# Kernel tuning notes

Measured on AMD Instinct MI355X. Metric: run time of the kernel, lower is better.

The kernel has to match this reference:

```python
import jax, jax.numpy as jnp
import numpy as np

NUM_HEADS = 12

def _pe(L, d):
    # standard sinusoidal positional encoding, shape (1, L, d)
    pos = jnp.arange(L, dtype=jnp.float32)[:, None]
    i = jnp.arange(d)[None, :]
    angle = pos / jnp.power(10000.0, (2 * (i // 2)).astype(jnp.float32) / d)
    pe = jnp.where(i % 2 == 0, jnp.sin(angle), jnp.cos(angle))
    return pe[None]

def _ln(x, scale, bias, eps=1e-5):
    m = x.mean(-1, keepdims=True)
    v = ((x - m) ** 2).mean(-1, keepdims=True)
    return (x - m) / jnp.sqrt(v + eps) * scale + bias

def setup_inputs() -> dict:
    key = jax.random.key(0)
    ks = jax.random.split(key, 8)
    D = 768
    s = 0.02
    return {
        "x": jax.random.normal(ks[0], (8, D, 32, 32), jnp.float32),
        "context_token": jax.random.normal(ks[1], (1, 1, D), jnp.float32),
        "register_tokens": jax.random.normal(ks[2], (1, 4, D), jnp.float32),
        "in_proj_w": jax.random.normal(ks[3], (3 * D, D), jnp.float32) * s,
        "in_proj_b": jnp.zeros((3 * D,), jnp.float32),
        "out_proj_w": jax.random.normal(ks[4], (D, D), jnp.float32) * s,
        "out_proj_b": jnp.zeros((D,), jnp.float32),
        "ln1_s": jnp.ones((D,), jnp.float32),
        "ln1_b": jnp.zeros((D,), jnp.float32),
        "ln2_s": jnp.ones((D,), jnp.float32),
        "ln2_b": jnp.zeros((D,), jnp.float32),
        "ffn_w1": jax.random.normal(ks[5], (4 * D, D), jnp.float32) * s,
        "ffn_b1": jnp.zeros((4 * D,), jnp.float32),
        "ffn_w2": jax.random.normal(ks[6], (D, 4 * D), jnp.float32) * s,
        "ffn_b2": jnp.zeros((D,), jnp.float32),
    }

def reference(x, context_token, register_tokens, in_proj_w, in_proj_b,
              out_proj_w, out_proj_b, ln1_s, ln1_b, ln2_s, ln2_b,
              ffn_w1, ffn_b1, ffn_w2, ffn_b2):
    B, d, h, w = x.shape
    N = h * w
    R = register_tokens.shape[1]
    G = 1 + R  # global tokens: context + registers
    nh = NUM_HEADS
    dh = d // nh
    # (B, N, d)
    x_flat = x.reshape(B, d, N).transpose(0, 2, 1)
    tokens = jnp.concatenate([
        jnp.broadcast_to(context_token, (B, 1, d)),
        jnp.broadcast_to(register_tokens, (B, R, d)),
    ], axis=1)
    tokens = tokens + _pe(G, d)
    xwt = _ln(jnp.concatenate([tokens, x_flat], axis=1), ln1_s, ln1_b)
    S = G + N
    # MultiheadAttention (eval mode, dropout off): fused in-projection
    qkv = xwt @ in_proj_w.T + in_proj_b
    q, k, v = jnp.split(qkv, 3, axis=-1)
    to_heads = lambda t: t.reshape(B, S, nh, dh).transpose(0, 2, 1, 3)
    q, k, v = to_heads(q), to_heads(k), to_heads(v)
    scores = jnp.einsum('bhqd,bhkd->bhqk', q, k) / np.float32(np.sqrt(dh))
    # mask (True = disallowed): feature rows (>=G) cannot attend to global cols (<G);
    # global rows attend everything; feature-feature block allowed.
    row_feat = jnp.arange(S) >= G
    col_glob = jnp.arange(S) < G
    disallowed = row_feat[:, None] & col_glob[None, :]
    scores = jnp.where(disallowed, -jnp.inf, scores)
    attn = jax.nn.softmax(scores, axis=-1)
    o = jnp.einsum('bhqk,bhkd->bhqd', attn, v).transpose(0, 2, 1, 3).reshape(B, S, d)
    o = o @ out_proj_w.T + out_proj_b
    y = o + xwt
    ff = jax.nn.gelu(_ln(y, ln2_s, ln2_b) @ ffn_w1.T + ffn_b1, approximate=False) @ ffn_w2.T + ffn_b2
    y = y + ff
    context_out = y[:, 0:1, :]
    register_out = y[:, 1:G, :]
    feature_out = y[:, G:, :].transpose(0, 2, 1).reshape(B, d, h, w)
    return feature_out, context_out, register_out
```

## Files before the change

### kernel.cpp

```cpp
#include <hip/hip_runtime.h>
#include <hip/hip_bf16.h>
#include <cmath>

typedef unsigned short u16;
typedef __bf16 bf16x8 __attribute__((ext_vector_type(8)));
typedef float floatx4 __attribute__((ext_vector_type(4)));

#define SQ 1029
#define DM 768
#define NH 12
#define SQP 1088
#define SSC 0.18033688011112042f

#define GLD16(gp, lp) __builtin_amdgcn_global_load_lds( \
    (const __attribute__((address_space(1))) unsigned int*)(gp), \
    (__attribute__((address_space(3))) unsigned int*)(lp), 16, 0, 0)

#define OFF_WQKV ((size_t)0)
#define OFF_WOUT ((size_t)3538944)
#define OFF_W1   ((size_t)4718592)
#define OFF_W2   ((size_t)9437184)
#define OFF_XF   ((size_t)14155776)
#define OFF_XWT  ((size_t)26800128)
#define OFF_QKV  ((size_t)39444480)
#define OFF_VT   ((size_t)77783040)
#define OFF_Y    ((size_t)91152384)
#define OFF_BQ   ((size_t)103796736)

__device__ __forceinline__ float bf2f(u16 u) {
  unsigned int x = ((unsigned int)u) << 16;
  float f; __builtin_memcpy(&f, &x, 4); return f;
}
__device__ __forceinline__ u16 f2bf(float f) {
  unsigned int x; __builtin_memcpy(&x, &f, 4);
  x = (x + 0x7fffu + ((x >> 16) & 1u)) >> 16;
  return (u16)x;
}
__device__ __forceinline__ unsigned int pk_bf16(float a, float b) {
  __hip_bfloat162 h = __float22bfloat162_rn(make_float2(a, b));
  unsigned int u; __builtin_memcpy(&u, &h, 4); return u;
}

__device__ __forceinline__ void blockReduce2(float& s1, float& s2) {
  #pragma unroll
  for (int o = 32; o > 0; o >>= 1) { s1 += __shfl_xor(s1, o); s2 += __shfl_xor(s2, o); }
  __shared__ float t1[4], t2[4];
  const int w = threadIdx.x >> 6;
  if ((threadIdx.x & 63) == 0) { t1[w] = s1; t2[w] = s2; }
  __syncthreads();
  s1 = t1[0] + t1[1] + t1[2] + t1[3];
  s2 = t2[0] + t2[1] + t2[2] + t2[3];
}

__global__ __launch_bounds__(256) void convw_all(
    const float* __restrict__ a, const float* __restrict__ b,
    const float* __restrict__ c, const float* __restrict__ d, u16* __restrict__ dst) {
  int i = blockIdx.x * 256 + threadIdx.x;
  if (i >= 1769472) return;
  const float* src; int off;
  if (i < 442368)       { src = a; off = i; }
  else if (i < 589824)  { src = b; off = i - 442368; }
  else if (i < 1179648) { src = c; off = i - 589824; }
  else                  { src = d; off = i - 1179648; }
  float4 v = ((const float4*)src)[off];
  if (i < 147456) { v.x *= SSC; v.y *= SSC; v.z *= SSC; v.w *= SSC; }
  ushort4 o; o.x = f2bf(v.x); o.y = f2bf(v.y); o.z = f2bf(v.z); o.w = f2bf(v.w);
  ((ushort4*)dst)[i] = o;
}

__global__ __launch_bounds__(256) void convb(const float* __restrict__ b, float* __restrict__ o) {
  int i = blockIdx.x * 256 + threadIdx.x;
  if (i >= 2304) return;
  o[i] = (i < 768) ? b[i] * SSC : b[i];
}

__global__ __launch_bounds__(256) void transpose_x(const float* __restrict__ x, u16* __restrict__ xf) {
  __shared__ u16 tile[32][33];
  const int b = blockIdx.x, ct = blockIdx.y, nt = blockIdx.z;
  const int i = threadIdx.x, jj = threadIdx.y;
  #pragma unroll
  for (int kk = 0; kk < 4; ++kk) {
    int j = jj + kk * 8;
    tile[j][i] = f2bf(x[((size_t)b * 768 + ct * 32 + j) * 1024 + nt * 32 + i]);
  }
  __syncthreads();
  #pragma unroll
  for (int kk = 0; kk < 4; ++kk) {
    int j = jj + kk * 8;
    xf[((size_t)b * 1024 + nt * 32 + j) * 768 + ct * 32 + i] = tile[i][j];
  }
}

__global__ __launch_bounds__(256) void build_xwt(
    const u16* __restrict__ xf, const float* __restrict__ ctx, const float* __restrict__ regt,
    const float* __restrict__ g, const float* __restrict__ be, u16* __restrict__ xwt) {
  const int row = blockIdx.x;
  const int b = row / SQ, s = row % SQ;
  const int tid = threadIdx.x;
  float v[3];
  #pragma unroll
  for (int i = 0; i < 3; ++i) {
    const int c = tid + i * 256;
    float val;
    if (s >= 5) {
      val = bf2f(xf[((size_t)b * 1024 + (s - 5)) * DM + c]);
    } else {
      float tok = (s == 0) ? ctx[c] : regt[(s - 1) * DM + c];
      float e = (float)(2 * (c / 2)) * (1.0f / 768.0f);
      float ang = (float)s / powf(10000.0f, e);
      val = tok + ((c & 1) ? cosf(ang) : sinf(ang));
    }
    v[i] = val;
  }
  float s1 = v[0] + v[1] + v[2];
  float s2 = v[0] * v[0] + v[1] * v[1] + v[2] * v[2];
  blockReduce2(s1, s2);
  const float mean = s1 * (1.0f / 768.0f);
  const float var = s2 * (1.0f / 768.0f) - mean * mean;
  const float rs = rsqrtf(fmaxf(var, 0.0f) + 1e-5f);
  #pragma unroll
  for (int i = 0; i < 3; ++i) {
    const int c = tid + i * 256;
    xwt[(size_t)row * DM + c] = f2bf((v[i] - mean) * rs * g[c] + be[c]);
  }
}

__global__ __launch_bounds__(256) void ln2k(
    const u16* __restrict__ y, const float* __restrict__ g, const float* __restrict__ be,
    u16* __restrict__ out) {
  const int row = blockIdx.x;
  const int tid = threadIdx.x;
  float v[3];
  #pragma unroll
  for (int i = 0; i < 3; ++i) v[i] = bf2f(y[(size_t)row * DM + tid + i * 256]);
  float s1 = v[0] + v[1] + v[2];
  float s2 = v[0] * v[0] + v[1] * v[1] + v[2] * v[2];
  blockReduce2(s1, s2);
  const float mean = s1 * (1.0f / 768.0f);
  const float var = s2 * (1.0f / 768.0f) - mean * mean;
  const float rs = rsqrtf(fmaxf(var, 0.0f) + 1e-5f);
  #pragma unroll
  for (int i = 0; i < 3; ++i) {
    const int c = tid + i * 256;
    out[(size_t)row * DM + c] = f2bf((v[i] - mean) * rs * g[c] + be[c]);
  }
}

template<int EPI, int K, int NB>
__global__ __launch_bounds__(256) void gemmk(
    const u16* __restrict__ A, const u16* __restrict__ W, const float* __restrict__ bias,
    const u16* __restrict__ res, u16* __restrict__ out, int M) {
  constexpr int N = NB * 128;
  __shared__ u16 SM[16384];
  u16* Asm = SM;
  u16* Bsm = SM + 8192;
  const int tid = threadIdx.x, wave = tid >> 6, lane = tid & 63, quad = lane >> 4, l16 = lane & 15;
  const int lin = blockIdx.x;
  constexpr int FULL = 64 * NB;
  int mb, nb;
  if (lin < FULL) { const int g = lin / (8 * NB); const int r = lin - g * 8 * NB; mb = g * 8 + (r & 7); nb = r >> 3; }
  else { mb = 64; nb = lin - FULL; }
  const int m0 = mb * 128, n0 = nb * 128;
  const int wm = wave & 1, wn = wave >> 1;

  const u16* Ap[4]; const u16* Wp[4]; u16* la[4]; u16* lb[4];
  #pragma unroll
  for (int it = 0; it < 4; ++it) {
    const int c = it * 256 + tid;
    const int row = c >> 3, gch = (c & 7) ^ (row & 7);
    Ap[it] = A + (size_t)min(m0 + row, M - 1) * K + gch * 8;
    Wp[it] = W + (size_t)(n0 + row) * K + gch * 8;
    la[it] = Asm + c * 8;
    lb[it] = Bsm + c * 8;
  }

  floatx4 acc[4][4];
  #pragma unroll
  for (int i = 0; i < 4; ++i)
    #pragma unroll
    for (int j = 0; j < 4; ++j) { floatx4 z = {0.f, 0.f, 0.f, 0.f}; acc[i][j] = z; }

  const int ch0 = (quad ^ (l16 & 7)) << 3;
  const int ch1 = ((4 + quad) ^ (l16 & 7)) << 3;

  #pragma unroll 1
  for (int ko = 0; ko < K / 768; ++ko) {
    #pragma unroll
    for (int ki = 0; ki < 768; ki += 64) {
      __syncthreads();
      #pragma unroll
      for (int it = 0; it < 4; ++it) GLD16(Ap[it] + ki, la[it]);
      #pragma unroll
      for (int it = 0; it < 4; ++it) GLD16(Wp[it] + ki, lb[it]);
      __syncthreads();
      #pragma unroll
      for (int kk = 0; kk < 2; ++kk) {
        const int ch = kk ? ch1 : ch0;
        bf16x8 a[4], b[4];
        #pragma unroll
        for (int i = 0; i < 4; ++i) a[i] = *(const bf16x8*)&Asm[(wm * 64 + i * 16 + l16) * 64 + ch];
        #pragma unroll
        for (int j = 0; j < 4; ++j) b[j] = *(const bf16x8*)&Bsm[(wn * 64 + j * 16 + l16) * 64 + ch];
        #pragma unroll
        for (int i = 0; i < 4; ++i)
          #pragma unroll
          for (int j = 0; j < 4; ++j)
            acc[i][j] = __builtin_amdgcn_mfma_f32_16x16x32_bf16(b[j], a[i], acc[i][j], 0, 0, 0);
      }
    }
    if (K > 768) {
      #pragma unroll
      for (int it = 0; it < 4; ++it) { Ap[it] += 768; Wp[it] += 768; }
    }
  }

  #pragma unroll
  for (int j = 0; j < 4; ++j) {
    const float4 b4 = *(const float4*)(bias + n0 + wn * 64 + j * 16 + quad * 4);
    #pragma unroll
    for (int i = 0; i < 4; ++i) {
      acc[i][j][0] += b4.x; acc[i][j][1] += b4.y; acc[i][j][2] += b4.z; acc[i][j][3] += b4.w;
    }
  }
  if constexpr (EPI == 2) {
    #pragma unroll
    for (int i = 0; i < 4; ++i)
      #pragma unroll
      for (int j = 0; j < 4; ++j)
        #pragma unroll
        for (int r = 0; r < 4; ++r) {
          const float v = acc[i][j][r];
          acc[i][j][r] = v / (1.0f + exp2f(-2.3022221f * (v + 0.044715f * v * v * v)));
        }
  }
  __syncthreads();
  u16* Ep = SM + wave * 2304;
  #pragma unroll
  for (int h = 0; h < 2; ++h) {
    #pragma unroll
    for (int i2 = 0; i2 < 2; ++i2) {
      const int i = h * 2 + i2;
      #pragma unroll
      for (int j = 0; j < 4; ++j) {
        uint2 w;
        w.x = pk_bf16(acc[i][j][0], acc[i][j][1]);
        w.y = pk_bf16(acc[i][j][2], acc[i][j][3]);
        *(uint2*)&Ep[(i2 * 16 + l16) * 72 + j * 16 + quad * 4] = w;
      }
    }
    #pragma unroll
    for (int s = 0; s < 4; ++s) {
      const int lrow = s * 8 + (lane >> 3);
      const int gm = m0 + wm * 64 + h * 32 + lrow;
      const int gn = n0 + wn * 64 + (lane & 7) * 8;
      uint4 lv = *(const uint4*)&Ep[lrow * 72 + (lane & 7) * 8];
      if constexpr (EPI == 1 || EPI == 3) {
        const uint4 rv = *(const uint4*)(res + (size_t)min(gm, M - 1) * N + gn);
        const unsigned* lp = &lv.x; const unsigned* rp = &rv.x;
        uint4 ov; unsigned* op = &ov.x;
        #pragma unroll
        for (int d = 0; d < 4; ++d) {
          const float a0 = bf2f((u16)(lp[d] & 0xffffu)) + bf2f((u16)(rp[d] & 0xffffu));
          const float a1 = bf2f((u16)(lp[d] >> 16)) + bf2f((u16)(rp[d] >> 16));
          op[d] = pk_bf16(a0, a1);
        }
        lv = ov;
      }
      if (gm < M) *(uint4*)(out + (size_t)gm * N + gn) = lv;
    }
  }
}

__global__ __launch_bounds__(256) void vtrans(const u16* __restrict__ qkv, u16* __restrict__ vt) {
  __shared__ u16 t[32][33];
  const int bh = blockIdx.x, st = blockIdx.y, dt = blockIdx.z;
  const int bq = bh / NH, hh = bh % NH;
  u16* vd = vt + (size_t)bh * 64 * SQP;
  const int i = threadIdx.x, jj = threadIdx.y;
  #pragma unroll
  for (int kk = 0; kk < 4; ++kk) {
    int j = jj + kk * 8;
    t[j][i] = qkv[(size_t)(bq * SQ + st * 32 + j) * 2304 + 1536 + hh * 64 + dt * 32 + i];
  }
  __syncthreads();
  #pragma unroll
  for (int kk = 0; kk < 4; ++kk) {
    int j = jj + kk * 8;
    vd[(size_t)(dt * 32 + j) * SQP + st * 32 + i] = t[i][j];
  }
}

__global__ __launch_bounds__(256) void attn_flash(
    const u16* __restrict__ qkv, const u16* __restrict__ vt, u16* __restrict__ out) {
  const int bh = blockIdx.x, qt = blockIdx.y;
  const int b = bh / NH, h = bh % NH;
  const int tid = threadIdx.x, wave = tid >> 6, lane = tid & 63, quad = lane >> 4, l16 = lane & 15;
  __shared__ u16 Qs[4096], Ks[4096], VTs[4096];
  __shared__ u16 Ps[64 * 72];
  const int q0 = qt * 64;
  const u16* qk = qkv + (size_t)b * SQ * 2304 + h * 64;
  const u16* vslab = vt + (size_t)bh * 64 * SQP;
  const int c0 = tid, c1 = tid + 256;
  const int r0 = c0 >> 3, q0c = (c0 & 7) ^ (r0 & 7);
  const int r1 = c1 >> 3, q1c = (c1 & 7) ^ (r1 & 7);
  u16* L0Q = Qs + wave * 512;  u16* L1Q = Qs + 2048 + wave * 512;
  u16* L0K = Ks + wave * 512;  u16* L1K = Ks + 2048 + wave * 512;
  u16* L0V = VTs + wave * 512; u16* L1V = VTs + 2048 + wave * 512;

  GLD16(qk + (size_t)(q0 + r0) * 2304 + q0c * 8, L0Q);
  GLD16(qk + (size_t)(q0 + r1) * 2304 + q1c * 8, L1Q);

  floatx4 Oa[4];
  #pragma unroll
  for (int nt = 0; nt < 4; ++nt) { floatx4 z = {0.f, 0.f, 0.f, 0.f}; Oa[nt] = z; }
  float l_acc = 0.f;
  const int qrow = wave * 16 + l16;
  const bool qfeat = (q0 + qrow >= 5);
  bf16x8 qf0, qf1;

  for (int t = 0; t < 17; ++t) {
    const int k0 = t * 64;
    __syncthreads();
    GLD16(qk + 768 + (size_t)(k0 + r0) * 2304 + q0c * 8, L0K);
    GLD16(qk + 768 + (size_t)(k0 + r1) * 2304 + q1c * 8, L1K);
    GLD16(vslab + (size_t)r0 * SQP + k0 + q0c * 8, L0V);
    GLD16(vslab + (size_t)r1 * SQP + k0 + q1c * 8, L1V);
    __syncthreads();

    if (t == 0) {
      qf0 = *(const bf16x8*)&Qs[qrow * 64 + ((quad ^ (qrow & 7)) << 3)];
      qf1 = *(const bf16x8*)&Qs[qrow * 64 + (((4 + quad) ^ (qrow & 7)) << 3)];
    }

    floatx4 st[4];
    #pragma unroll
    for (int mt = 0; mt < 4; ++mt) { floatx4 z = {0.f, 0.f, 0.f, 0.f}; st[mt] = z; }
    #pragma unroll
    for (int kk = 0; kk < 2; ++kk) {
      const bf16x8 qf = kk ? qf1 : qf0;
      #pragma unroll
      for (int mt = 0; mt < 4; ++mt) {
        const int krow = mt * 16 + l16;
        bf16x8 kf = *(const bf16x8*)&Ks[krow * 64 + (((kk * 4 + quad) ^ (krow & 7)) << 3)];
        st[mt] = __builtin_amdgcn_mfma_f32_16x16x32_bf16(kf, qf, st[mt], 0, 0, 0);
      }
    }

    if (t == 16) {
      float p[4];
      #pragma unroll
      for (int r = 0; r < 4; ++r) {
        float pv = exp2f(st[0][r]);
        p[r] = (quad * 4 + r < 5) ? pv : 0.f;
      }
      l_acc += (p[0] + p[1]) + (p[2] + p[3]);
      uint2 w;
      w.x = pk_bf16(p[0], p[1]);
      w.y = pk_bf16(p[2], p[3]);
      *(uint2*)&Ps[qrow * 72 + quad * 4] = w;
      const uint2 zz = {0u, 0u};
      #pragma unroll
      for (int mt = 1; mt < 4; ++mt) *(uint2*)&Ps[qrow * 72 + mt * 16 + quad * 4] = zz;
    } else if (t == 0) {
      #pragma unroll
      for (int mt = 0; mt < 4; ++mt) {
        float p[4];
        #pragma unroll
        for (int r = 0; r < 4; ++r) {
          float pv = exp2f(st[mt][r]);
          if (mt == 0) pv = (qfeat && (quad * 4 + r < 5)) ? 0.f : pv;
          p[r] = pv;
        }
        l_acc += (p[0] + p[1]) + (p[2] + p[3]);
        uint2 w;
        w.x = pk_bf16(p[0], p[1]);
        w.y = pk_bf16(p[2], p[3]);
        *(uint2*)&Ps[qrow * 72 + mt * 16 + quad * 4] = w;
      }
    } else {
      #pragma unroll
      for (int mt = 0; mt < 4; ++mt) {
        float p[4];
        #pragma unroll
        for (int r = 0; r < 4; ++r) p[r] = exp2f(st[mt][r]);
        l_acc += (p[0] + p[1]) + (p[2] + p[3]);
        uint2 w;
        w.x = pk_bf16(p[0], p[1]);
        w.y = pk_bf16(p[2], p[3]);
        *(uint2*)&Ps[qrow * 72 + mt * 16 + quad * 4] = w;
      }
    }

    auto pv_step = [&](int kk) {
      bf16x8 pf = *(const bf16x8*)&Ps[qrow * 72 + kk * 32 + quad * 8];
      #pragma unroll
      for (int nt = 0; nt < 4; ++nt) {
        const int brow = nt * 16 + l16;
        bf16x8 bb = *(const bf16x8*)&VTs[brow * 64 + (((kk * 4 + quad) ^ (brow & 7)) << 3)];
        Oa[nt] = __builtin_amdgcn_mfma_f32_16x16x32_bf16(pf, bb, Oa[nt], 0, 0, 0);
      }
    };
    pv_step(0);
    if (t != 16) pv_step(1);
  }

  float lt = l_acc;
  lt += __shfl_xor(lt, 16);
  lt += __shfl_xor(lt, 32);
  lt = fmaxf(lt, 1e-30f);
  #pragma unroll
  for (int nt = 0; nt < 4; ++nt)
    #pragma unroll
    for (int r = 0; r < 4; ++r) {
      const int qo = quad * 4 + r;
      const float lr = __shfl(lt, (lane & 48) | qo);
      const int qg2 = q0 + wave * 16 + qo;
      if (qg2 < SQ)
        out[((size_t)b * SQ + qg2) * DM + h * 64 + nt * 16 + l16] = f2bf(Oa[nt][r] / lr);
    }
}

__global__ __launch_bounds__(256) void transpose_out(const u16* __restrict__ yf, float* __restrict__ out) {
  __shared__ u16 tile[32][33];
  const int b = blockIdx.x, nt = blockIdx.y, ct = blockIdx.z;
  const int i = threadIdx.x, jj = threadIdx.y;
  #pragma unroll
  for (int kk = 0; kk < 4; ++kk) {
    int j = jj + kk * 8;
    tile[j][i] = yf[((size_t)b * SQ + 5 + nt * 32 + j) * DM + ct * 32 + i];
  }
  __syncthreads();
  #pragma unroll
  for (int kk = 0; kk < 4; ++kk) {
    int j = jj + kk * 8;
    out[((size_t)b * 768 + ct * 32 + j) * 1024 + nt * 32 + i] = bf2f(tile[i][j]);
  }
}

__global__ __launch_bounds__(256) void out_small(const u16* __restrict__ yf, float* __restrict__ out) {
  const int idx = blockIdx.x * 256 + threadIdx.x;
  if (idx >= 8 * 5 * DM) return;
  const int b = idx / (5 * DM);
  const int r = idx % (5 * DM);
  const int s = r / DM, c = r % DM;
  const float v = bf2f(yf[((size_t)b * SQ + s) * DM + c]);
  if (s == 0) out[(size_t)6291456 + (size_t)b * DM + c] = v;
  else out[(size_t)6291456 + 6144 + ((size_t)b * 4 + (s - 1)) * DM + c] = v;
}

extern "C" void kernel_launch(void* const* d_in, const int* in_sizes, int n_in,
                              void* d_out, int out_size, void* d_ws, size_t ws_size,
                              hipStream_t stream) {
  const float* x    = (const float*)d_in[0];
  const float* ctx  = (const float*)d_in[1];
  const float* regt = (const float*)d_in[2];
  const float* wqkv = (const float*)d_in[3];
  const float* bqkv = (const float*)d_in[4];
  const float* wout = (const float*)d_in[5];
  const float* bout = (const float*)d_in[6];
  const float* ln1s = (const float*)d_in[7];
  const float* ln1b = (const float*)d_in[8];
  const float* ln2s = (const float*)d_in[9];
  const float* ln2b = (const float*)d_in[10];
  const float* w1   = (const float*)d_in[11];
  const float* b1   = (const float*)d_in[12];
  const float* w2   = (const float*)d_in[13];
  const float* b2   = (const float*)d_in[14];

  char* ws = (char*)d_ws;
  u16* wb_all = (u16*)(ws + OFF_WQKV);
  u16* wqkv_b = (u16*)(ws + OFF_WQKV);
  u16* wout_b = (u16*)(ws + OFF_WOUT);
  u16* w1_b   = (u16*)(ws + OFF_W1);
  u16* w2_b   = (u16*)(ws + OFF_W2);
  u16* xf     = (u16*)(ws + OFF_XF);
  u16* xwt    = (u16*)(ws + OFF_XWT);
  u16* qkv    = (u16*)(ws + OFF_QKV);
  u16* vtb    = (u16*)(ws + OFF_VT);
  u16* yb     = (u16*)(ws + OFF_Y);
  float* bqs  = (float*)(ws + OFF_BQ);
  u16* attnb  = (u16*)(ws + OFF_XF);
  u16* ynorm  = (u16*)(ws + OFF_XF);
  u16* h1     = (u16*)(ws + OFF_QKV);
  u16* yfin   = (u16*)(ws + OFF_XWT);
  float* outp = (float*)d_out;

  convw_all   <<<6912, 256, 0, stream>>>(wqkv, wout, w1, w2, wb_all);
  convb       <<<9, 256, 0, stream>>>(bqkv, bqs);
  transpose_x <<<dim3(8, 24, 32), dim3(32, 8), 0, stream>>>(x, xf);
  build_xwt   <<<8232, 256, 0, stream>>>(xf, ctx, regt, ln1s, ln1b, xwt);
  gemmk<0, 768, 18><<<65 * 18, 256, 0, stream>>>(xwt, wqkv_b, bqs, nullptr, qkv, 8232);
  vtrans      <<<dim3(96, 34, 2), dim3(32, 8), 0, stream>>>(qkv, vtb);
  attn_flash  <<<dim3(96, 17), 256, 0, stream>>>(qkv, vtb, attnb);
  gemmk<1, 768, 6><<<65 * 6, 256, 0, stream>>>(attnb, wout_b, bout, xwt, yb, 8232);
  ln2k        <<<8232, 256, 0, stream>>>(yb, ln2s, ln2b, ynorm);
  gemmk<2, 768, 24><<<65 * 24, 256, 0, stream>>>(ynorm, w1_b, b1, nullptr, h1, 8232);
  gemmk<3, 3072, 6><<<65 * 6, 256, 0, stream>>>(h1, w2_b, b2, yb, yfin, 8232);
  transpose_out<<<dim3(8, 32, 24), dim3(32, 8), 0, stream>>>(yfin, outp);
  out_small   <<<120, 256, 0, stream>>>(yfin, outp);
}
```

Measured before the change: 399.1 us.

## Add 256x256-tile 512-thread GEMM with 4-stage LDS pipeline for QKV and FFN1

Adds a new GEMM kernel using 256x256 output tiles, 8 waves per block, a 4-slot direct-to-LDS load pipeline and 128 KB dynamic shared memory. It replaces the 128-wide tile kernel for the QKV projection and the first FFN layer. The larger tiles raise arithmetic intensity and cut redundant global loads. The cost is fewer blocks, hence worse wave quantization across CUs, and higher register and LDS pressure that may limit occupancy.

```diff
diff --git a/kernel.cpp b/kernel.cpp
--- a/kernel.cpp
+++ b/kernel.cpp
@@ -252,6 +252,133 @@
     for (int s = 0; s < 4; ++s) {
       const int lrow = s * 8 + (lane >> 3);
       const int gm = m0 + wm * 64 + h * 32 + lrow;
+      const int gn = n0 + wn * 64 + (lane & 7) * 8;
+      uint4 lv = *(const uint4*)&Ep[lrow * 72 + (lane & 7) * 8];
+      if constexpr (EPI == 1 || EPI == 3) {
+        const uint4 rv = *(const uint4*)(res + (size_t)min(gm, M - 1) * N + gn);
+        const unsigned* lp = &lv.x; const unsigned* rp = &rv.x;
+        uint4 ov; unsigned* op = &ov.x;
+        #pragma unroll
+        for (int d = 0; d < 4; ++d) {
+          const float a0 = bf2f((u16)(lp[d] & 0xffffu)) + bf2f((u16)(rp[d] & 0xffffu));
+          const float a1 = bf2f((u16)(lp[d] >> 16)) + bf2f((u16)(rp[d] >> 16));
+          op[d] = pk_bf16(a0, a1);
+        }
+        lv = ov;
+      }
+      if (gm < M) *(uint4*)(out + (size_t)gm * N + gn) = lv;
+    }
+  }
+}
+
+template<int EPI, int K, int NB>
+__global__ __launch_bounds__(512, 2) void gemm256(
+    const u16* __restrict__ A, const u16* __restrict__ W, const float* __restrict__ bias,
+    const u16* __restrict__ res, u16* __restrict__ out, int M) {
+  constexpr int N = NB * 256;
+  constexpr int NT = K / 32;
+  extern __shared__ __align__(16) char SMb[];
+  const int tid = threadIdx.x, wave = tid >> 6, lane = tid & 63, quad = lane >> 4, l16 = lane & 15;
+  const int wm = wave >> 2, wn = wave & 3;
+  const int lin = blockIdx.x;
+  int mb, nb;
+  if (lin < 32 * NB) { const int g = lin / (8 * NB); const int r = lin - g * 8 * NB; mb = g * 8 + (r & 7); nb = r >> 3; }
+  else { mb = 32; nb = lin - 32 * NB; }
+  const int m0 = mb * 256, n0 = nb * 256;
+
+  const u16* Ag[2]; const u16* Wg[2];
+  #pragma unroll
+  for (int it = 0; it < 2; ++it) {
+    const int c = it * 512 + tid;
+    const int row = c >> 2;
+    const int k8 = (c & 3) ^ (row & 3);
+    Ag[it] = A + (size_t)min(m0 + row, M - 1) * K + k8 * 8;
+    Wg[it] = W + (size_t)(n0 + row) * K + k8 * 8;
+  }
+  const int ldst = tid * 16;
+
+  floatx4 acc[8][4];
+  #pragma unroll
+  for (int i = 0; i < 8; ++i)
+    #pragma unroll
+    for (int j = 0; j < 4; ++j) { floatx4 z = {0.f, 0.f, 0.f, 0.f}; acc[i][j] = z; }
+
+  const int aoff = ((wm * 128 + l16) * 32 + ((quad ^ (l16 & 3)) << 3)) * 2;
+  const int boff = 65536 + ((wn * 64 + l16) * 32 + ((quad ^ (l16 & 3)) << 3)) * 2;
+
+  auto STAGE = [&](int ts, int slot) {
+    const size_t ko = (size_t)ts * 32;
+    char* ab = SMb + slot * 16384 + ldst;
+    char* bb = SMb + 65536 + slot * 16384 + ldst;
+    GLD16(Ag[0] + ko, ab);
+    GLD16(Ag[1] + ko, ab + 8192);
+    GLD16(Wg[0] + ko, bb);
+    GLD16(Wg[1] + ko, bb + 8192);
+  };
+
+  STAGE(0, 0); STAGE(1, 1); STAGE(2, 2);
+
+  #pragma unroll 1
+  for (int t = 0; t < NT; ++t) {
+    asm volatile("s_waitcnt vmcnt(8)" ::: "memory");
+    __builtin_amdgcn_s_barrier();
+    __builtin_amdgcn_sched_barrier(0);
+    STAGE(t + 3 < NT ? t + 3 : NT - 1, (t + 3) & 3);
+    const char* base = SMb + (t & 3) * 16384;
+    bf16x8 a[8], b[4];
+    #pragma unroll
+    for (int i = 0; i < 8; ++i) a[i] = *(const bf16x8*)(base + aoff + i * 1024);
+    #pragma unroll
+    for (int j = 0; j < 4; ++j) b[j] = *(const bf16x8*)(base + boff + j * 1024);
+    __builtin_amdgcn_s_setprio(1);
+    #pragma unroll
+    for (int i = 0; i < 8; ++i)
+      #pragma unroll
+      for (int j = 0; j < 4; ++j)
+        acc[i][j] = __builtin_amdgcn_mfma_f32_16x16x32_bf16(b[j], a[i], acc[i][j], 0, 0, 0);
+    __builtin_amdgcn_s_setprio(0);
+  }
+
+  asm volatile("s_waitcnt vmcnt(0)" ::: "memory");
+  __builtin_amdgcn_s_barrier();
+
+  #pragma unroll
+  for (int j = 0; j < 4; ++j) {
+    const float4 b4 = *(const float4*)(bias + n0 + wn * 64 + j * 16 + quad * 4);
+    #pragma unroll
+    for (int i = 0; i < 8; ++i) {
+      acc[i][j][0] += b4.x; acc[i][j][1] += b4.y; acc[i][j][2] += b4.z; acc[i][j][3] += b4.w;
+    }
+  }
+  if constexpr (EPI == 2) {
+    #pragma unroll
+    for (int i = 0; i < 8; ++i)
+      #pragma unroll
+      for (int j = 0; j < 4; ++j)
+        #pragma unroll
+        for (int r = 0; r < 4; ++r) {
+          const float v = acc[i][j][r];
+          acc[i][j][r] = v / (1.0f + exp2f(-2.3022221f * (v + 0.044715f * v * v * v)));
+        }
+  }
+  u16* Ep = (u16*)SMb + wave * 2304;
+  #pragma unroll
+  for (int g = 0; g < 4; ++g) {
+    #pragma unroll
+    for (int i2 = 0; i2 < 2; ++i2) {
+      const int i = g * 2 + i2;
+      #pragma unroll
+      for (int j = 0; j < 4; ++j) {
+        uint2 w;
+        w.x = pk_bf16(acc[i][j][0], acc[i][j][1]);
+        w.y = pk_bf16(acc[i][j][2], acc[i][j][3]);
+        *(uint2*)&Ep[(i2 * 16 + l16) * 72 + j * 16 + quad * 4] = w;
+      }
+    }
+    #pragma unroll
+    for (int s = 0; s < 4; ++s) {
+      const int lrow = s * 8 + (lane >> 3);
+      const int gm = m0 + wm * 128 + g * 32 + lrow;
       const int gn = n0 + wn * 64 + (lane & 7) * 8;
       uint4 lv = *(const uint4*)&Ep[lrow * 72 + (lane & 7) * 8];
       if constexpr (EPI == 1 || EPI == 3) {
@@ -485,16 +612,25 @@
   u16* yfin   = (u16*)(ws + OFF_XWT);
   float* outp = (float*)d_out;
 
+  static bool attr_done = false;
+  if (!attr_done) {
+    attr_done = true;
+    hipFuncSetAttribute(reinterpret_cast<const void*>(&gemm256<0, 768, 9>),
+                        hipFuncAttributeMaxDynamicSharedMemorySize, 131072);
+    hipFuncSetAttribute(reinterpret_cast<const void*>(&gemm256<2, 768, 12>),
+                        hipFuncAttributeMaxDynamicSharedMemorySize, 131072);
+  }
+
   convw_all   <<<6912, 256, 0, stream>>>(wqkv, wout, w1, w2, wb_all);
   convb       <<<9, 256, 0, stream>>>(bqkv, bqs);
   transpose_x <<<dim3(8, 24, 32), dim3(32, 8), 0, stream>>>(x, xf);
   build_xwt   <<<8232, 256, 0, stream>>>(xf, ctx, regt, ln1s, ln1b, xwt);
-  gemmk<0, 768, 18><<<65 * 18, 256, 0, stream>>>(xwt, wqkv_b, bqs, nullptr, qkv, 8232);
+  gemm256<0, 768, 9><<<33 * 9, 512, 131072, stream>>>(xwt, wqkv_b, bqs, nullptr, qkv, 8232);
   vtrans      <<<dim3(96, 34, 2), dim3(32, 8), 0, stream>>>(qkv, vtb);
   attn_flash  <<<dim3(96, 17), 256, 0, stream>>>(qkv, vtb, attnb);
   gemmk<1, 768, 6><<<65 * 6, 256, 0, stream>>>(attnb, wout_b, bout, xwt, yb, 8232);
   ln2k        <<<8232, 256, 0, stream>>>(yb, ln2s, ln2b, ynorm);
-  gemmk<2, 768, 24><<<65 * 24, 256, 0, stream>>>(ynorm, w1_b, b1, nullptr, h1, 8232);
+  gemm256<2, 768, 12><<<33 * 12, 512, 131072, stream>>>(ynorm, w1_b, b1, nullptr, h1, 8232);
   gemmk<3, 3072, 6><<<65 * 6, 256, 0, stream>>>(h1, w2_b, b2, yb, yfin, 8232);
   transpose_out<<<dim3(8, 32, 24), dim3(32, 8), 0, stream>>>(yfin, outp);
   out_small   <<<120, 256, 0, stream>>>(yfin, outp);
```

Result: slower. 412.8 us (+3.4%).

## Replace 128x128 GEMM with 256x256-tile double-buffered 8-wave GEMM

Applied to the files above, without the earlier changes.

Replaces the 128x128-tile, 4-wave, single-buffered GEMM with a 256x256-tile, 8-wave kernel that uses 128KB of dynamic LDS. Global-to-LDS loads for the next k-tiles are issued two stages ahead, waited on with explicit vmcnt counts, and MFMA sections are raised in priority with setprio. The goal is more data reuse per tile and overlap of memory loads with compute. The trade-off is far fewer blocks per GEMM (e.g. 99 for the out-projection and FFN2 GEMMs), which can leave many CUs idle on a large GPU and worsens tail effects from the partial last M tile.

```diff
diff --git a/kernel.cpp b/kernel.cpp
--- a/kernel.cpp
+++ b/kernel.cpp
@@ -147,84 +147,100 @@
 }
 
 template<int EPI, int K, int NB>
-__global__ __launch_bounds__(256) void gemmk(
+__global__ __launch_bounds__(512, 2) void gemm256(
     const u16* __restrict__ A, const u16* __restrict__ W, const float* __restrict__ bias,
     const u16* __restrict__ res, u16* __restrict__ out, int M) {
-  constexpr int N = NB * 128;
-  __shared__ u16 SM[16384];
-  u16* Asm = SM;
-  u16* Bsm = SM + 8192;
+  constexpr int N = NB * 256;
+  constexpr int NT = K / 64;
+  extern __shared__ __align__(16) char SMb[];
   const int tid = threadIdx.x, wave = tid >> 6, lane = tid & 63, quad = lane >> 4, l16 = lane & 15;
+  const int wm = wave >> 2, wn = wave & 3;
   const int lin = blockIdx.x;
-  constexpr int FULL = 64 * NB;
   int mb, nb;
-  if (lin < FULL) { const int g = lin / (8 * NB); const int r = lin - g * 8 * NB; mb = g * 8 + (r & 7); nb = r >> 3; }
-  else { mb = 64; nb = lin - FULL; }
-  const int m0 = mb * 128, n0 = nb * 128;
-  const int wm = wave & 1, wn = wave >> 1;
-
-  const u16* Ap[4]; const u16* Wp[4]; u16* la[4]; u16* lb[4];
+  if (lin < 32 * NB) { const int g = lin / (8 * NB); const int r = lin - g * 8 * NB; mb = g * 8 + (r & 7); nb = r >> 3; }
+  else { mb = 32; nb = lin - 32 * NB; }
+  const int m0 = mb * 256, n0 = nb * 256;
+
+  const u16* Ap[4]; const u16* Wp[4];
   #pragma unroll
   for (int it = 0; it < 4; ++it) {
-    const int c = it * 256 + tid;
+    const int c = it * 512 + tid;
     const int row = c >> 3, gch = (c & 7) ^ (row & 7);
     Ap[it] = A + (size_t)min(m0 + row, M - 1) * K + gch * 8;
     Wp[it] = W + (size_t)(n0 + row) * K + gch * 8;
-    la[it] = Asm + c * 8;
-    lb[it] = Bsm + c * 8;
-  }
-
-  floatx4 acc[4][4];
-  #pragma unroll
-  for (int i = 0; i < 4; ++i)
+  }
+  char* asl = SMb + tid * 16;
+  char* bsl = SMb + 65536 + tid * 16;
+
+  auto STAGE = [&](int ts, int slot) {
+    const int ko = ts * 64;
+    #pragma unroll
+    for (int it = 0; it < 4; ++it) GLD16(Ap[it] + ko, asl + slot * 32768 + it * 8192);
+    #pragma unroll
+    for (int it = 0; it < 4; ++it) GLD16(Wp[it] + ko, bsl + slot * 32768 + it * 8192);
+  };
+
+  floatx4 acc[8][4];
+  #pragma unroll
+  for (int i = 0; i < 8; ++i)
     #pragma unroll
     for (int j = 0; j < 4; ++j) { floatx4 z = {0.f, 0.f, 0.f, 0.f}; acc[i][j] = z; }
 
   const int ch0 = (quad ^ (l16 & 7)) << 3;
   const int ch1 = ((4 + quad) ^ (l16 & 7)) << 3;
 
+  STAGE(0, 0); STAGE(1, 1);
+
   #pragma unroll 1
-  for (int ko = 0; ko < K / 768; ++ko) {
-    #pragma unroll
-    for (int ki = 0; ki < 768; ki += 64) {
-      __syncthreads();
-      #pragma unroll
-      for (int it = 0; it < 4; ++it) GLD16(Ap[it] + ki, la[it]);
-      #pragma unroll
-      for (int it = 0; it < 4; ++it) GLD16(Wp[it] + ki, lb[it]);
-      __syncthreads();
-      #pragma unroll
-      for (int kk = 0; kk < 2; ++kk) {
-        const int ch = kk ? ch1 : ch0;
-        bf16x8 a[4], b[4];
-        #pragma unroll
-        for (int i = 0; i < 4; ++i) a[i] = *(const bf16x8*)&Asm[(wm * 64 + i * 16 + l16) * 64 + ch];
-        #pragma unroll
-        for (int j = 0; j < 4; ++j) b[j] = *(const bf16x8*)&Bsm[(wn * 64 + j * 16 + l16) * 64 + ch];
-        #pragma unroll
-        for (int i = 0; i < 4; ++i)
-          #pragma unroll
-          for (int j = 0; j < 4; ++j)
-            acc[i][j] = __builtin_amdgcn_mfma_f32_16x16x32_bf16(b[j], a[i], acc[i][j], 0, 0, 0);
-      }
-    }
-    if (K > 768) {
-      #pragma unroll
-      for (int it = 0; it < 4; ++it) { Ap[it] += 768; Wp[it] += 768; }
-    }
+  for (int t = 0; t < NT; ++t) {
+    if (t < NT - 1) { asm volatile("s_waitcnt vmcnt(8)" ::: "memory"); }
+    else            { asm volatile("s_waitcnt vmcnt(0)" ::: "memory"); }
+    __builtin_amdgcn_s_barrier();
+    __builtin_amdgcn_sched_barrier(0);
+    const u16* As = (const u16*)(SMb + (t & 1) * 32768);
+    const u16* Bs = (const u16*)(SMb + 65536 + (t & 1) * 32768);
+    bf16x8 a0[8], b0[4], a1[8], b1[4];
+    #pragma unroll
+    for (int i = 0; i < 8; ++i) a0[i] = *(const bf16x8*)&As[(wm * 128 + i * 16 + l16) * 64 + ch0];
+    #pragma unroll
+    for (int j = 0; j < 4; ++j) b0[j] = *(const bf16x8*)&Bs[(wn * 64 + j * 16 + l16) * 64 + ch0];
+    __builtin_amdgcn_s_setprio(1);
+    #pragma unroll
+    for (int i = 0; i < 8; ++i)
+      #pragma unroll
+      for (int j = 0; j < 4; ++j)
+        acc[i][j] = __builtin_amdgcn_mfma_f32_16x16x32_bf16(b0[j], a0[i], acc[i][j], 0, 0, 0);
+    __builtin_amdgcn_s_setprio(0);
+    #pragma unroll
+    for (int i = 0; i < 8; ++i) a1[i] = *(const bf16x8*)&As[(wm * 128 + i * 16 + l16) * 64 + ch1];
+    #pragma unroll
+    for (int j = 0; j < 4; ++j) b1[j] = *(const bf16x8*)&Bs[(wn * 64 + j * 16 + l16) * 64 + ch1];
+    asm volatile("s_waitcnt lgkmcnt(0)" ::: "memory");
+    __builtin_amdgcn_sched_barrier(0);
+    __builtin_amdgcn_s_barrier();
+    __builtin_amdgcn_sched_barrier(0);
+    if (t + 2 < NT) STAGE(t + 2, t & 1);
+    __builtin_amdgcn_sched_barrier(0);
+    __builtin_amdgcn_s_setprio(1);
+    #pragma unroll
+    for (int i = 0; i < 8; ++i)
+      #pragma unroll
+      for (int j = 0; j < 4; ++j)
+        acc[i][j] = __builtin_amdgcn_mfma_f32_16x16x32_bf16(b1[j], a1[i], acc[i][j], 0, 0, 0);
+    __builtin_amdgcn_s_setprio(0);
   }
 
   #pragma unroll
   for (int j = 0; j < 4; ++j) {
     const float4 b4 = *(const float4*)(bias + n0 + wn * 64 + j * 16 + quad * 4);
     #pragma unroll
-    for (int i = 0; i < 4; ++i) {
+    for (int i = 0; i < 8; ++i) {
       acc[i][j][0] += b4.x; acc[i][j][1] += b4.y; acc[i][j][2] += b4.z; acc[i][j][3] += b4.w;
     }
   }
   if constexpr (EPI == 2) {
     #pragma unroll
-    for (int i = 0; i < 4; ++i)
+    for (int i = 0; i < 8; ++i)
       #pragma unroll
       for (int j = 0; j < 4; ++j)
         #pragma unroll
@@ -233,13 +249,12 @@
           acc[i][j][r] = v / (1.0f + exp2f(-2.3022221f * (v + 0.044715f * v * v * v)));
         }
   }
-  __syncthreads();
-  u16* Ep = SM + wave * 2304;
-  #pragma unroll
-  for (int h = 0; h < 2; ++h) {
+  u16* Ep = (u16*)SMb + wave * 2304;
+  #pragma unroll
+  for (int g = 0; g < 4; ++g) {
     #pragma unroll
     for (int i2 = 0; i2 < 2; ++i2) {
-      const int i = h * 2 + i2;
+      const int i = g * 2 + i2;
       #pragma unroll
       for (int j = 0; j < 4; ++j) {
         uint2 w;
@@ -251,7 +266,7 @@
     #pragma unroll
     for (int s = 0; s < 4; ++s) {
       const int lrow = s * 8 + (lane >> 3);
-      const int gm = m0 + wm * 64 + h * 32 + lrow;
+      const int gm = m0 + wm * 128 + g * 32 + lrow;
       const int gn = n0 + wn * 64 + (lane & 7) * 8;
       uint4 lv = *(const uint4*)&Ep[lrow * 72 + (lane & 7) * 8];
       if constexpr (EPI == 1 || EPI == 3) {
@@ -485,17 +500,30 @@
   u16* yfin   = (u16*)(ws + OFF_XWT);
   float* outp = (float*)d_out;
 
+  static bool attr_done = false;
+  if (!attr_done) {
+    attr_done = true;
+    hipFuncSetAttribute(reinterpret_cast<const void*>(&gemm256<0, 768, 9>),
+                        hipFuncAttributeMaxDynamicSharedMemorySize, 131072);
+    hipFuncSetAttribute(reinterpret_cast<const void*>(&gemm256<1, 768, 3>),
+                        hipFuncAttributeMaxDynamicSharedMemorySize, 131072);
+    hipFuncSetAttribute(reinterpret_cast<const void*>(&gemm256<2, 768, 12>),
+                        hipFuncAttributeMaxDynamicSharedMemorySize, 131072);
+    hipFuncSetAttribute(reinterpret_cast<const void*>(&gemm256<3, 3072, 3>),
+                        hipFuncAttributeMaxDynamicSharedMemorySize, 131072);
+  }
+
   convw_all   <<<6912, 256, 0, stream>>>(wqkv, wout, w1, w2, wb_all);
   convb       <<<9, 256, 0, stream>>>(bqkv, bqs);
   transpose_x <<<dim3(8, 24, 32), dim3(32, 8), 0, stream>>>(x, xf);
   build_xwt   <<<8232, 256, 0, stream>>>(xf, ctx, regt, ln1s, ln1b, xwt);
-  gemmk<0, 768, 18><<<65 * 18, 256, 0, stream>>>(xwt, wqkv_b, bqs, nullptr, qkv, 8232);
+  gemm256<0, 768, 9><<<33 * 9, 512, 131072, stream>>>(xwt, wqkv_b, bqs, nullptr, qkv, 8232);
   vtrans      <<<dim3(96, 34, 2), dim3(32, 8), 0, stream>>>(qkv, vtb);
   attn_flash  <<<dim3(96, 17), 256, 0, stream>>>(qkv, vtb, attnb);
-  gemmk<1, 768, 6><<<65 * 6, 256, 0, stream>>>(attnb, wout_b, bout, xwt, yb, 8232);
+  gemm256<1, 768, 3><<<33 * 3, 512, 131072, stream>>>(attnb, wout_b, bout, xwt, yb, 8232);
   ln2k        <<<8232, 256, 0, stream>>>(yb, ln2s, ln2b, ynorm);
-  gemmk<2, 768, 24><<<65 * 24, 256, 0, stream>>>(ynorm, w1_b, b1, nullptr, h1, 8232);
-  gemmk<3, 3072, 6><<<65 * 6, 256, 0, stream>>>(h1, w2_b, b2, yb, yfin, 8232);
+  gemm256<2, 768, 12><<<33 * 12, 512, 131072, stream>>>(ynorm, w1_b, b1, nullptr, h1, 8232);
+  gemm256<3, 3072, 3><<<33 * 3, 512, 131072, stream>>>(h1, w2_b, b2, yb, yfin, 8232);
   transpose_out<<<dim3(8, 32, 24), dim3(32, 8), 0, stream>>>(yfin, outp);
   out_small   <<<120, 256, 0, stream>>>(yfin, outp);
 }
```

New measurement: 439.3 us. +10.1%, slower.

## Fuse input transpose with LayerNorm1 and fold bias conversion into weight kernel

Applied to the files above, without the earlier changes.

Replaces the separate transpose-to-bf16 kernel and the per-row LayerNorm kernel with one kernel that loads a 32-token slab of x, transposes it in shared memory and normalizes each row with wave-level reductions. This drops the bf16 intermediate round trip through global memory. Global tokens get their own small kernel, and the q-bias scaling is merged into the weight-conversion kernel to save a launch. The fused kernel uses about 49KB of LDS per block and runs only 256 blocks, which may limit occupancy.

```diff
diff --git a/kernel.cpp b/kernel.cpp
--- a/kernel.cpp
+++ b/kernel.cpp
@@ -54,9 +54,17 @@
 
 __global__ __launch_bounds__(256) void convw_all(
     const float* __restrict__ a, const float* __restrict__ b,
-    const float* __restrict__ c, const float* __restrict__ d, u16* __restrict__ dst) {
+    const float* __restrict__ c, const float* __restrict__ d,
+    const float* __restrict__ bq, u16* __restrict__ dst, float* __restrict__ bqs) {
   int i = blockIdx.x * 256 + threadIdx.x;
-  if (i >= 1769472) return;
+  if (i >= 1770048) return;
+  if (i >= 1769472) {
+    const int off = i - 1769472;
+    float4 v = ((const float4*)bq)[off];
+    if (off < 192) { v.x *= SSC; v.y *= SSC; v.z *= SSC; v.w *= SSC; }
+    ((float4*)bqs)[off] = v;
+    return;
+  }
   const float* src; int off;
   if (i < 442368)       { src = a; off = i; }
   else if (i < 589824)  { src = b; off = i - 442368; }
@@ -68,49 +76,20 @@
   ((ushort4*)dst)[i] = o;
 }
 
-__global__ __launch_bounds__(256) void convb(const float* __restrict__ b, float* __restrict__ o) {
-  int i = blockIdx.x * 256 + threadIdx.x;
-  if (i >= 2304) return;
-  o[i] = (i < 768) ? b[i] * SSC : b[i];
-}
-
-__global__ __launch_bounds__(256) void transpose_x(const float* __restrict__ x, u16* __restrict__ xf) {
-  __shared__ u16 tile[32][33];
-  const int b = blockIdx.x, ct = blockIdx.y, nt = blockIdx.z;
-  const int i = threadIdx.x, jj = threadIdx.y;
-  #pragma unroll
-  for (int kk = 0; kk < 4; ++kk) {
-    int j = jj + kk * 8;
-    tile[j][i] = f2bf(x[((size_t)b * 768 + ct * 32 + j) * 1024 + nt * 32 + i]);
-  }
-  __syncthreads();
-  #pragma unroll
-  for (int kk = 0; kk < 4; ++kk) {
-    int j = jj + kk * 8;
-    xf[((size_t)b * 1024 + nt * 32 + j) * 768 + ct * 32 + i] = tile[i][j];
-  }
-}
-
-__global__ __launch_bounds__(256) void build_xwt(
-    const u16* __restrict__ xf, const float* __restrict__ ctx, const float* __restrict__ regt,
+__global__ __launch_bounds__(256) void build_tok(
+    const float* __restrict__ ctx, const float* __restrict__ regt,
     const float* __restrict__ g, const float* __restrict__ be, u16* __restrict__ xwt) {
   const int row = blockIdx.x;
-  const int b = row / SQ, s = row % SQ;
+  const int b = row / 5, s = row % 5;
   const int tid = threadIdx.x;
   float v[3];
   #pragma unroll
   for (int i = 0; i < 3; ++i) {
     const int c = tid + i * 256;
-    float val;
-    if (s >= 5) {
-      val = bf2f(xf[((size_t)b * 1024 + (s - 5)) * DM + c]);
-    } else {
-      float tok = (s == 0) ? ctx[c] : regt[(s - 1) * DM + c];
-      float e = (float)(2 * (c / 2)) * (1.0f / 768.0f);
-      float ang = (float)s / powf(10000.0f, e);
-      val = tok + ((c & 1) ? cosf(ang) : sinf(ang));
-    }
-    v[i] = val;
+    float tok = (s == 0) ? ctx[c] : regt[(s - 1) * DM + c];
+    float e = (float)(2 * (c / 2)) * (1.0f / 768.0f);
+    float ang = (float)s / powf(10000.0f, e);
+    v[i] = tok + ((c & 1) ? cosf(ang) : sinf(ang));
   }
   float s1 = v[0] + v[1] + v[2];
   float s2 = v[0] * v[0] + v[1] * v[1] + v[2] * v[2];
@@ -121,7 +100,49 @@
   #pragma unroll
   for (int i = 0; i < 3; ++i) {
     const int c = tid + i * 256;
-    xwt[(size_t)row * DM + c] = f2bf((v[i] - mean) * rs * g[c] + be[c]);
+    xwt[((size_t)b * SQ + s) * DM + c] = f2bf((v[i] - mean) * rs * g[c] + be[c]);
+  }
+}
+
+__global__ __launch_bounds__(256) void ln1_fused(
+    const float* __restrict__ x, const float* __restrict__ g, const float* __restrict__ be,
+    u16* __restrict__ xwt) {
+  __shared__ u16 XT[32][772];
+  const int b = blockIdx.x >> 5, st = blockIdx.x & 31;
+  const int tid = threadIdx.x;
+  const int i2 = tid & 15, cj = tid >> 4;
+  const int n0 = st * 32;
+  #pragma unroll 4
+  for (int ct = 0; ct < 48; ++ct) {
+    const int c = ct * 16 + cj;
+    const float2 v = *(const float2*)&x[((size_t)b * 768 + c) * 1024 + n0 + i2 * 2];
+    XT[i2 * 2][c]     = f2bf(v.x);
+    XT[i2 * 2 + 1][c] = f2bf(v.y);
+  }
+  __syncthreads();
+  const int wave = tid >> 6, lane = tid & 63;
+  float gr[12], br[12];
+  #pragma unroll
+  for (int k = 0; k < 12; ++k) { gr[k] = g[lane + k * 64]; br[k] = be[lane + k * 64]; }
+  #pragma unroll
+  for (int rr = 0; rr < 8; ++rr) {
+    const int row = wave * 8 + rr;
+    float v[12];
+    float s1 = 0.f, s2 = 0.f;
+    #pragma unroll
+    for (int k = 0; k < 12; ++k) {
+      v[k] = bf2f(XT[row][lane + k * 64]);
+      s1 += v[k]; s2 += v[k] * v[k];
+    }
+    #pragma unroll
+    for (int o = 32; o > 0; o >>= 1) { s1 += __shfl_xor(s1, o); s2 += __shfl_xor(s2, o); }
+    const float mean = s1 * (1.0f / 768.0f);
+    const float var = s2 * (1.0f / 768.0f) - mean * mean;
+    const float rs = rsqrtf(fmaxf(var, 0.0f) + 1e-5f);
+    u16* dst = xwt + ((size_t)b * SQ + 5 + n0 + row) * DM;
+    #pragma unroll
+    for (int k = 0; k < 12; ++k)
+      dst[lane + k * 64] = f2bf((v[k] - mean) * rs * gr[k] + br[k]);
   }
 }
 
@@ -473,7 +494,6 @@
   u16* wout_b = (u16*)(ws + OFF_WOUT);
   u16* w1_b   = (u16*)(ws + OFF_W1);
   u16* w2_b   = (u16*)(ws + OFF_W2);
-  u16* xf     = (u16*)(ws + OFF_XF);
   u16* xwt    = (u16*)(ws + OFF_XWT);
   u16* qkv    = (u16*)(ws + OFF_QKV);
   u16* vtb    = (u16*)(ws + OFF_VT);
@@ -485,10 +505,9 @@
   u16* yfin   = (u16*)(ws + OFF_XWT);
   float* outp = (float*)d_out;
 
-  convw_all   <<<6912, 256, 0, stream>>>(wqkv, wout, w1, w2, wb_all);
-  convb       <<<9, 256, 0, stream>>>(bqkv, bqs);
-  transpose_x <<<dim3(8, 24, 32), dim3(32, 8), 0, stream>>>(x, xf);
-  build_xwt   <<<8232, 256, 0, stream>>>(xf, ctx, regt, ln1s, ln1b, xwt);
+  convw_all   <<<6915, 256, 0, stream>>>(wqkv, wout, w1, w2, bqkv, wb_all, bqs);
+  build_tok   <<<40, 256, 0, stream>>>(ctx, regt, ln1s, ln1b, xwt);
+  ln1_fused   <<<256, 256, 0, stream>>>(x, ln1s, ln1b, xwt);
   gemmk<0, 768, 18><<<65 * 18, 256, 0, stream>>>(xwt, wqkv_b, bqs, nullptr, qkv, 8232);
   vtrans      <<<dim3(96, 34, 2), dim3(32, 8), 0, stream>>>(qkv, vtb);
   attn_flash  <<<dim3(96, 17), 256, 0, stream>>>(qkv, vtb, attnb);
```

Result: no change. 395.3 us (-0.9%).
